# Performance work log

Measured on AMD Instinct MI355X. Metric: run time of the kernel, lower is better.

Reference implementation:

```python
import jax, jax.numpy as jnp
import numpy as np
import math

B, L, H, E, D = 4, 1024, 8, 64, 64


def setup_inputs() -> dict:
    key = jax.random.key(0)
    kq, kk, kv, ks = jax.random.split(key, 4)
    return {
        "queries": jax.random.normal(kq, (B, L, H, E), dtype=jnp.float32),
        "keys": jax.random.normal(kk, (B, L, H, E), dtype=jnp.float32),
        "values": jax.random.normal(kv, (B, L, H, D), dtype=jnp.float32),
        "sigma": jax.random.normal(ks, (B, L, H), dtype=jnp.float32),
    }


def reference(queries, keys, values, sigma):
    b, l, h, e = queries.shape
    scale = 1.0 / math.sqrt(e)

    # scores: [B, H, L, S]
    scores = jnp.einsum("blhe,bshe->bhls", queries, keys)

    # triangular causal mask (strict upper triangle -> -inf), applied BEFORE scaling
    causal = jnp.triu(jnp.ones((l, l), dtype=bool), k=1)  # [L, L]
    scores = jnp.where(causal[None, None], -jnp.inf, scores)
    attn = scale * scores

    # sigma branch: [B, L, H] -> [B, H, L], sigmoid/pow transform, broadcast over S
    sg = jax.nn.sigmoid(jnp.transpose(sigma, (0, 2, 1)) * 5.0) + 1e-5
    sg = jnp.power(3.0, sg) - 1.0          # [B, H, L]
    sg = sg[..., None]                      # [B, H, L, 1] (broadcast instead of tile)

    # Gaussian prior from |i - j| distances
    idx = jnp.arange(l, dtype=jnp.float32)
    dist = jnp.abs(idx[:, None] - idx[None, :])  # [L, L]
    prior = (1.0 / (math.sqrt(2.0 * math.pi) * sg)) * jnp.exp(-(dist ** 2) / (2.0 * sg ** 2))  # [B,H,L,L]

    series = jax.nn.softmax(attn, axis=-1)  # dropout rate 0.0 -> identity
    V = jnp.einsum("bhls,bshd->blhd", series, values)

    sigma_out = jnp.broadcast_to(sg, prior.shape)  # matches tf.tile semantics
    return (V, series, prior, sigma_out)
```

## Files before the change

kernel.cpp:

```cpp
#include <hip/hip_runtime.h>
#include <hip/hip_bf16.h>

#define NB 4
#define NL 1024
#define NH 8
#define NE 64
#define NPRIOR (NB * NH * NL)

typedef __bf16 bf16x8_t __attribute__((ext_vector_type(8)));
typedef __bf16 bf16x4_t __attribute__((ext_vector_type(4)));
typedef float f32x4_t __attribute__((ext_vector_type(4)));

__device__ __forceinline__ int kidx(int row, int col) {
    return (row << 6) + (col ^ ((row & 7) << 3));
}
__device__ __forceinline__ int pidx(int row, int col) {
    return (row << 10) + (col ^ ((row & 7) << 3));
}

#define BAR() do { asm volatile("s_waitcnt lgkmcnt(0)" ::: "memory"); \
                   __builtin_amdgcn_s_barrier();                      \
                   asm volatile("" ::: "memory"); } while (0)

__global__ __launch_bounds__(256) void fused_kernel(
    const float* __restrict__ Qg, const float* __restrict__ Kg,
    const float* __restrict__ Vg, const float* __restrict__ Sgm,
    float* __restrict__ outV, float* __restrict__ outSer,
    float* __restrict__ outP, float* __restrict__ outSig)
{
    __shared__ __bf16 Pl[32 * 1024];
    __shared__ __bf16 KV[64 * 64];
    __shared__ float rsum[4][16];
    __shared__ float rinvs[32];
    __shared__ float sgl[72], cstl[72], nil[72];

    const int bid = blockIdx.x;
    const int p  = bid & 31;
    const int jp = bid >> 5;
    const int h = p & 7, b = p >> 3;
    const int tid = threadIdx.x;
    const int lane = tid & 63, wave = tid >> 6;
    const int l16 = lane & 15, lq = lane >> 4;
    const int rg  = wave >> 1;
    const int nsb = (wave & 1) << 1;
    const int rowstride = NH * NE;

    const float* Qb = Qg + ((size_t)b * NL) * rowstride + h * NE;
    const float* Kb = Kg + ((size_t)b * NL) * rowstride + h * NE;
    const float* Vb = Vg + ((size_t)b * NL) * rowstride + h * NE;
    float* ser = outSer + ((size_t)p << 20);
    const float scale = 0.125f;

    if (tid < 72) {
        const int g = (bid << 6) + tid;
        if (g < NPRIOR) {
            const int i  = g & (NL - 1);
            const int ph = g >> 10;
            const float s   = Sgm[((size_t)(ph >> 3) * NL + i) * NH + (ph & 7)];
            const float sig = 1.f / (1.f + __expf(-5.f * s)) + 1e-5f;
            const float sg  = expm1f(sig * 1.0986122886681098f);
            sgl[tid]  = sg;
            cstl[tid] = 0.3989422804014327f / sg;
            nil[tid]  = -0.5f / (sg * sg);
        }
    }

    int prow = 0;
    auto emit4 = [&]() {
        #pragma unroll
        for (int c = 0; c < 4; ++c) {
            const int lr = prow + c;
            const int g  = (bid << 6) + lr;
            if (g < NPRIOR) {
                const int i  = g & (NL - 1);
                const int ph = g >> 10;
                const float sg  = sgl[lr];
                const float cst = cstl[lr];
                const float ni  = nil[lr];
                const size_t ob = ((size_t)ph << 20) + ((size_t)i << 10);
                const int j0 = tid << 2;
                const float fd = (float)(i - j0);
                f32x4_t pr;
                pr.x = cst * __expf(fd * fd * ni);
                const float f1 = fd - 1.f; pr.y = cst * __expf(f1 * f1 * ni);
                const float f2 = fd - 2.f; pr.z = cst * __expf(f2 * f2 * ni);
                const float f3 = fd - 3.f; pr.w = cst * __expf(f3 * f3 * ni);
                __builtin_nontemporal_store(pr, (f32x4_t*)(outP + ob + j0));
                f32x4_t sv = {sg, sg, sg, sg};
                __builtin_nontemporal_store(sv, (f32x4_t*)(outSig + ob + j0));
            }
        }
        prow += 4;
    };

    float4 kr[8];
    auto loadK = [&](int ct) {
        #pragma unroll
        for (int nn = 0; nn < 2; ++nn) {
            const float* row = Kb +
                (size_t)((ct << 6) + ((nsb + nn) << 4) + l16) * rowstride;
            kr[nn * 4 + 0] = *(const float4*)(row + (lq << 3));
            kr[nn * 4 + 1] = *(const float4*)(row + (lq << 3) + 4);
            kr[nn * 4 + 2] = *(const float4*)(row + 32 + (lq << 3));
            kr[nn * 4 + 3] = *(const float4*)(row + 32 + (lq << 3) + 4);
        }
    };

    float4 preV[4];
    auto loadV = [&](int ct) {
        const float* src = Vb + ((size_t)(ct << 6)) * rowstride;
        #pragma unroll
        for (int it = 0; it < 4; ++it) {
            int g = tid + (it << 8);
            int row = g >> 4, c4 = (g & 15) << 2;
            preV[it] = *(const float4*)(src + (size_t)row * rowstride + c4);
        }
    };
    auto writeVt = [&]() {
        #pragma unroll
        for (int it = 0; it < 4; ++it) {
            int g = tid + (it << 8);
            int row = g >> 4, c4 = (g & 15) << 2;
            KV[kidx(c4 + 0, row)] = (__bf16)preV[it].x;
            KV[kidx(c4 + 1, row)] = (__bf16)preV[it].y;
            KV[kidx(c4 + 2, row)] = (__bf16)preV[it].z;
            KV[kidx(c4 + 3, row)] = (__bf16)preV[it].w;
        }
    };

    auto do_tile = [&](int t) {
        const int r0  = t << 5;
        const int nct = (t + 2) >> 1;

        loadK(0);
        loadV(0);

        BAR();
        #pragma unroll
        for (int it = 0; it < 2; ++it) {
            int g = tid + (it << 8);
            int row = g >> 4, c4 = (g & 15) << 2;
            float4 v = *(const float4*)(Qb + (size_t)(r0 + row) * rowstride + c4);
            bf16x4_t w;
            w[0] = (__bf16)v.x; w[1] = (__bf16)v.y;
            w[2] = (__bf16)v.z; w[3] = (__bf16)v.w;
            *(bf16x4_t*)(KV + kidx(row, c4)) = w;
        }
        BAR();
        bf16x8_t qf0, qf1;
        {
            int row = (rg << 4) + l16;
            qf0 = *(bf16x8_t*)(KV + kidx(row, lq << 3));
            qf1 = *(bf16x8_t*)(KV + kidx(row, 32 + (lq << 3)));
        }

        const int qloc = (rg << 4) + l16;
        const int qg   = r0 + qloc;
        const int rloc0 = (rg << 4) + (lq << 2);

        float psum = 0.f;
        f32x4_t accO0 = {0.f, 0.f, 0.f, 0.f};
        f32x4_t accO1 = {0.f, 0.f, 0.f, 0.f};

        for (int ct = 0; ct < nct; ++ct) {
            BAR();
            writeVt();
            if (ct + 1 < nct) loadV(ct + 1);
            #pragma unroll
            for (int nn = 0; nn < 2; ++nn) {
                bf16x8_t a0, a1;
                {
                    float4 p0 = kr[nn * 4 + 0], p1 = kr[nn * 4 + 1];
                    float4 p2 = kr[nn * 4 + 2], p3 = kr[nn * 4 + 3];
                    a0[0] = (__bf16)p0.x; a0[1] = (__bf16)p0.y;
                    a0[2] = (__bf16)p0.z; a0[3] = (__bf16)p0.w;
                    a0[4] = (__bf16)p1.x; a0[5] = (__bf16)p1.y;
                    a0[6] = (__bf16)p1.z; a0[7] = (__bf16)p1.w;
                    a1[0] = (__bf16)p2.x; a1[1] = (__bf16)p2.y;
                    a1[2] = (__bf16)p2.z; a1[3] = (__bf16)p2.w;
                    a1[4] = (__bf16)p3.x; a1[5] = (__bf16)p3.y;
                    a1[6] = (__bf16)p3.z; a1[7] = (__bf16)p3.w;
                }
                f32x4_t acc = {0.f, 0.f, 0.f, 0.f};
                acc = __builtin_amdgcn_mfma_f32_16x16x32_bf16(a0, qf0, acc, 0, 0, 0);
                acc = __builtin_amdgcn_mfma_f32_16x16x32_bf16(a1, qf1, acc, 0, 0, 0);
                const int jbase = (ct << 6) + ((nsb + nn) << 4) + (lq << 2);
                bf16x4_t pw;
                #pragma unroll
                for (int r = 0; r < 4; ++r) {
                    float e = (jbase + r <= qg) ? __expf(acc[r] * scale) : 0.f;
                    psum += e;
                    pw[r] = (__bf16)e;
                }
                *(bf16x4_t*)(Pl + pidx(qloc, jbase)) = pw;
            }
            if (ct + 1 < nct) loadK(ct + 1);
            BAR();
            #pragma unroll
            for (int ks = 0; ks < 2; ++ks) {
                bf16x8_t pa = *(bf16x8_t*)(Pl + pidx((rg << 4) + l16,
                                             (ct << 6) + (ks << 5) + (lq << 3)));
                bf16x8_t vb0 = *(bf16x8_t*)(KV + kidx((nsb << 4) + l16,
                                             (ks << 5) + (lq << 3)));
                accO0 = __builtin_amdgcn_mfma_f32_16x16x32_bf16(pa, vb0, accO0, 0, 0, 0);
                bf16x8_t vb1 = *(bf16x8_t*)(KV + kidx(((nsb + 1) << 4) + l16,
                                             (ks << 5) + (lq << 3)));
                accO1 = __builtin_amdgcn_mfma_f32_16x16x32_bf16(pa, vb1, accO1, 0, 0, 0);
            }
            emit4();
        }

        {
            float s = psum;
            s += __shfl_xor(s, 16);
            s += __shfl_xor(s, 32);
            if (lane < 16) rsum[wave][l16] = s;
        }
        BAR();
        if (tid < 32) {
            int rgx = tid >> 4;
            float tot = rsum[rgx << 1][tid & 15] + rsum[(rgx << 1) | 1][tid & 15];
            rinvs[tid] = 1.f / tot;
        }
        BAR();

        #pragma unroll
        for (int r = 0; r < 4; ++r) {
            int rloc = rloc0 + r;
            float rv = rinvs[rloc];
            float* dst = outV + ((size_t)b * NL + r0 + rloc) * rowstride + h * NE;
            dst[(nsb << 4) + l16]       = accO0[r] * rv;
            dst[((nsb + 1) << 4) + l16] = accO1[r] * rv;
        }

        const int lim = nct << 6;
        #pragma unroll 2
        for (int rr = wave; rr < 32; rr += 4) {
            float rv = rinvs[rr];
            float* dst = ser + ((size_t)(r0 + rr) << 10);
            #pragma unroll
            for (int k = 0; k < 4; ++k) {
                int col = (lane << 2) + (k << 8);
                f32x4_t o;
                if (col < lim) {
                    bf16x4_t p4 = *(bf16x4_t*)(Pl + pidx(rr, col));
                    o.x = (float)p4[0] * rv;
                    o.y = (float)p4[1] * rv;
                    o.z = (float)p4[2] * rv;
                    o.w = (float)p4[3] * rv;
                } else {
                    o.x = 0.f; o.y = 0.f; o.z = 0.f; o.w = 0.f;
                }
                __builtin_nontemporal_store(o, (f32x4_t*)(dst + col));
            }
        }
    };

    do_tile(31 - jp);
    do_tile(jp);

    while (prow < 64) emit4();
}

extern "C" void kernel_launch(void* const* d_in, const int* in_sizes, int n_in,
                              void* d_out, int out_size, void* d_ws, size_t ws_size,
                              hipStream_t stream) {
    const float* Q  = (const float*)d_in[0];
    const float* K  = (const float*)d_in[1];
    const float* V  = (const float*)d_in[2];
    const float* Sg = (const float*)d_in[3];

    float* out      = (float*)d_out;
    float* outV     = out;
    float* outSer   = out + 2097152;
    float* outPrior = out + 35651584;
    float* outSig   = out + 69206016;

    hipLaunchKernelGGL(fused_kernel, dim3(512), dim3(256), 0, stream,
                       Q, K, V, Sg, outV, outSer, outPrior, outSig);
}
```

Measured before the change: 87.26 us.

## Split softmax into a row-sum pass and a streaming normalize pass to shrink LDS

A first pass computes only the softmax denominators with QK MFMAs. A second pass recomputes the scores and streams the normalized probabilities per 64-column tile straight to global memory. This removes the 64KB full-row P buffer in shared memory, which should allow more blocks per CU. The grid doubles to 1024 blocks with one 32-row tile each instead of paired tiles, and the prior/sigma rows are spread evenly across blocks. The cost is computing QK twice, and the per-block work is no longer balanced by the causal-pair trick.

```diff
diff --git a/kernel.cpp b/kernel.cpp
--- a/kernel.cpp
+++ b/kernel.cpp
@@ -14,8 +14,12 @@
 __device__ __forceinline__ int kidx(int row, int col) {
     return (row << 6) + (col ^ ((row & 7) << 3));
 }
-__device__ __forceinline__ int pidx(int row, int col) {
-    return (row << 10) + (col ^ ((row & 7) << 3));
+
+__device__ __forceinline__ bf16x8_t cvt8(const float4& a, const float4& b) {
+    bf16x8_t r;
+    r[0] = (__bf16)a.x; r[1] = (__bf16)a.y; r[2] = (__bf16)a.z; r[3] = (__bf16)a.w;
+    r[4] = (__bf16)b.x; r[5] = (__bf16)b.y; r[6] = (__bf16)b.z; r[7] = (__bf16)b.w;
+    return r;
 }
 
 #define BAR() do { asm volatile("s_waitcnt lgkmcnt(0)" ::: "memory"); \
@@ -28,15 +32,15 @@
     float* __restrict__ outV, float* __restrict__ outSer,
     float* __restrict__ outP, float* __restrict__ outSig)
 {
-    __shared__ __bf16 Pl[32 * 1024];
-    __shared__ __bf16 KV[64 * 64];
+    __shared__ __bf16 Vt[64 * 64];
+    __shared__ __bf16 Ps[32 * 64];
     __shared__ float rsum[4][16];
     __shared__ float rinvs[32];
-    __shared__ float sgl[72], cstl[72], nil[72];
+    __shared__ float sgl[32], cstl[32], nil[32];
 
     const int bid = blockIdx.x;
-    const int p  = bid & 31;
-    const int jp = bid >> 5;
+    const int p = bid & 31;
+    const int t = bid >> 5;
     const int h = p & 7, b = p >> 3;
     const int tid = threadIdx.x;
     const int lane = tid & 63, wave = tid >> 6;
@@ -50,61 +54,114 @@
     const float* Vb = Vg + ((size_t)b * NL) * rowstride + h * NE;
     float* ser = outSer + ((size_t)p << 20);
     const float scale = 0.125f;
-
-    if (tid < 72) {
-        const int g = (bid << 6) + tid;
-        if (g < NPRIOR) {
+    const int r0  = t << 5;
+    const int nct = (t + 2) >> 1;
+
+    if (tid < 32) {
+        const int g  = (bid << 5) + tid;
+        const int i  = g & (NL - 1);
+        const int ph = g >> 10;
+        const float s   = Sgm[((size_t)(ph >> 3) * NL + i) * NH + (ph & 7)];
+        const float sig = 1.f / (1.f + __expf(-5.f * s)) + 1e-5f;
+        const float sg  = expm1f(sig * 1.0986122886681098f);
+        sgl[tid]  = sg;
+        cstl[tid] = 0.3989422804014327f / sg;
+        nil[tid]  = -0.5f / (sg * sg);
+    }
+
+    int prow = 0;
+    auto emit2 = [&]() {
+        #pragma unroll
+        for (int c = 0; c < 2; ++c) {
+            const int lr = prow + c;
+            const int g  = (bid << 5) + lr;
             const int i  = g & (NL - 1);
             const int ph = g >> 10;
-            const float s   = Sgm[((size_t)(ph >> 3) * NL + i) * NH + (ph & 7)];
-            const float sig = 1.f / (1.f + __expf(-5.f * s)) + 1e-5f;
-            const float sg  = expm1f(sig * 1.0986122886681098f);
-            sgl[tid]  = sg;
-            cstl[tid] = 0.3989422804014327f / sg;
-            nil[tid]  = -0.5f / (sg * sg);
-        }
-    }
-
-    int prow = 0;
-    auto emit4 = [&]() {
-        #pragma unroll
-        for (int c = 0; c < 4; ++c) {
-            const int lr = prow + c;
-            const int g  = (bid << 6) + lr;
-            if (g < NPRIOR) {
-                const int i  = g & (NL - 1);
-                const int ph = g >> 10;
-                const float sg  = sgl[lr];
-                const float cst = cstl[lr];
-                const float ni  = nil[lr];
-                const size_t ob = ((size_t)ph << 20) + ((size_t)i << 10);
-                const int j0 = tid << 2;
-                const float fd = (float)(i - j0);
-                f32x4_t pr;
-                pr.x = cst * __expf(fd * fd * ni);
-                const float f1 = fd - 1.f; pr.y = cst * __expf(f1 * f1 * ni);
-                const float f2 = fd - 2.f; pr.z = cst * __expf(f2 * f2 * ni);
-                const float f3 = fd - 3.f; pr.w = cst * __expf(f3 * f3 * ni);
-                __builtin_nontemporal_store(pr, (f32x4_t*)(outP + ob + j0));
-                f32x4_t sv = {sg, sg, sg, sg};
-                __builtin_nontemporal_store(sv, (f32x4_t*)(outSig + ob + j0));
-            }
-        }
-        prow += 4;
-    };
-
-    float4 kr[8];
-    auto loadK = [&](int ct) {
+            const float sg  = sgl[lr];
+            const float cst = cstl[lr];
+            const float ni  = nil[lr];
+            const size_t ob = ((size_t)ph << 20) + ((size_t)i << 10);
+            const int j0 = tid << 2;
+            const float fd = (float)(i - j0);
+            f32x4_t pr;
+            pr.x = cst * __expf(fd * fd * ni);
+            const float f1 = fd - 1.f; pr.y = cst * __expf(f1 * f1 * ni);
+            const float f2 = fd - 2.f; pr.z = cst * __expf(f2 * f2 * ni);
+            const float f3 = fd - 3.f; pr.w = cst * __expf(f3 * f3 * ni);
+            __builtin_nontemporal_store(pr, (f32x4_t*)(outP + ob + j0));
+            f32x4_t sv = {sg, sg, sg, sg};
+            __builtin_nontemporal_store(sv, (f32x4_t*)(outSig + ob + j0));
+        }
+        prow += 2;
+    };
+
+    const int qloc = (rg << 4) + l16;
+    const int qg   = r0 + qloc;
+    bf16x8_t qf0, qf1;
+    {
+        const float* qr = Qb + (size_t)(r0 + qloc) * rowstride;
+        float4 a = *(const float4*)(qr + (lq << 3));
+        float4 c = *(const float4*)(qr + (lq << 3) + 4);
+        qf0 = cvt8(a, c);
+        float4 d = *(const float4*)(qr + 32 + (lq << 3));
+        float4 e = *(const float4*)(qr + 32 + (lq << 3) + 4);
+        qf1 = cvt8(d, e);
+    }
+
+    auto loadK = [&](int ct, bf16x8_t (&ka)[4]) {
         #pragma unroll
         for (int nn = 0; nn < 2; ++nn) {
-            const float* row = Kb +
+            const float* krow = Kb +
                 (size_t)((ct << 6) + ((nsb + nn) << 4) + l16) * rowstride;
-            kr[nn * 4 + 0] = *(const float4*)(row + (lq << 3));
-            kr[nn * 4 + 1] = *(const float4*)(row + (lq << 3) + 4);
-            kr[nn * 4 + 2] = *(const float4*)(row + 32 + (lq << 3));
-            kr[nn * 4 + 3] = *(const float4*)(row + 32 + (lq << 3) + 4);
-        }
-    };
+            float4 p0 = *(const float4*)(krow + (lq << 3));
+            float4 p1 = *(const float4*)(krow + (lq << 3) + 4);
+            float4 p2 = *(const float4*)(krow + 32 + (lq << 3));
+            float4 p3 = *(const float4*)(krow + 32 + (lq << 3) + 4);
+            ka[nn * 2 + 0] = cvt8(p0, p1);
+            ka[nn * 2 + 1] = cvt8(p2, p3);
+        }
+    };
+
+    auto qk_psum = [&](int ct, bf16x8_t (&ka)[4], float& ps) {
+        #pragma unroll
+        for (int nn = 0; nn < 2; ++nn) {
+            f32x4_t acc = {0.f, 0.f, 0.f, 0.f};
+            acc = __builtin_amdgcn_mfma_f32_16x16x32_bf16(ka[nn * 2 + 0], qf0, acc, 0, 0, 0);
+            acc = __builtin_amdgcn_mfma_f32_16x16x32_bf16(ka[nn * 2 + 1], qf1, acc, 0, 0, 0);
+            const int jb = (ct << 6) + ((nsb + nn) << 4) + (lq << 2);
+            #pragma unroll
+            for (int r = 0; r < 4; ++r)
+                if (jb + r <= qg) ps += __expf(acc[r] * scale);
+        }
+    };
+
+    float psum = 0.f;
+    {
+        bf16x8_t kA[4], kB[4];
+        loadK(0, kA);
+        #pragma unroll 1
+        for (int ct = 0; ct < nct; ct += 2) {
+            if (ct + 1 < nct) loadK(ct + 1, kB);
+            qk_psum(ct, kA, psum);
+            if (ct + 1 < nct) {
+                if (ct + 2 < nct) loadK(ct + 2, kA);
+                qk_psum(ct + 1, kB, psum);
+            }
+        }
+    }
+    psum += __shfl_xor(psum, 16);
+    psum += __shfl_xor(psum, 32);
+    if (lane < 16) rsum[wave][l16] = psum;
+    BAR();
+    if (tid < 32) {
+        const int rgx = tid >> 4;
+        float tot = rsum[rgx << 1][tid & 15] + rsum[(rgx << 1) | 1][tid & 15];
+        rinvs[tid] = 1.f / tot;
+    }
+    BAR();
+
+    f32x4_t accO0 = {0.f, 0.f, 0.f, 0.f};
+    f32x4_t accO1 = {0.f, 0.f, 0.f, 0.f};
 
     float4 preV[4];
     auto loadV = [&](int ct) {
@@ -121,145 +178,84 @@
         for (int it = 0; it < 4; ++it) {
             int g = tid + (it << 8);
             int row = g >> 4, c4 = (g & 15) << 2;
-            KV[kidx(c4 + 0, row)] = (__bf16)preV[it].x;
-            KV[kidx(c4 + 1, row)] = (__bf16)preV[it].y;
-            KV[kidx(c4 + 2, row)] = (__bf16)preV[it].z;
-            KV[kidx(c4 + 3, row)] = (__bf16)preV[it].w;
-        }
-    };
-
-    auto do_tile = [&](int t) {
-        const int r0  = t << 5;
-        const int nct = (t + 2) >> 1;
-
-        loadK(0);
-        loadV(0);
-
-        BAR();
-        #pragma unroll
-        for (int it = 0; it < 2; ++it) {
-            int g = tid + (it << 8);
-            int row = g >> 4, c4 = (g & 15) << 2;
-            float4 v = *(const float4*)(Qb + (size_t)(r0 + row) * rowstride + c4);
-            bf16x4_t w;
-            w[0] = (__bf16)v.x; w[1] = (__bf16)v.y;
-            w[2] = (__bf16)v.z; w[3] = (__bf16)v.w;
-            *(bf16x4_t*)(KV + kidx(row, c4)) = w;
-        }
-        BAR();
-        bf16x8_t qf0, qf1;
-        {
-            int row = (rg << 4) + l16;
-            qf0 = *(bf16x8_t*)(KV + kidx(row, lq << 3));
-            qf1 = *(bf16x8_t*)(KV + kidx(row, 32 + (lq << 3)));
-        }
-
-        const int qloc = (rg << 4) + l16;
-        const int qg   = r0 + qloc;
-        const int rloc0 = (rg << 4) + (lq << 2);
-
-        float psum = 0.f;
-        f32x4_t accO0 = {0.f, 0.f, 0.f, 0.f};
-        f32x4_t accO1 = {0.f, 0.f, 0.f, 0.f};
-
-        for (int ct = 0; ct < nct; ++ct) {
+            Vt[kidx(c4 + 0, row)] = (__bf16)preV[it].x;
+            Vt[kidx(c4 + 1, row)] = (__bf16)preV[it].y;
+            Vt[kidx(c4 + 2, row)] = (__bf16)preV[it].z;
+            Vt[kidx(c4 + 3, row)] = (__bf16)preV[it].w;
+        }
+    };
+
+    bf16x8_t kc[4];
+    loadK(0, kc);
+    loadV(0);
+
+    const int srow = tid >> 3;
+    const int scol = (tid & 7) << 3;
+
+    #pragma unroll 1
+    for (int ct = 0; ct < 16; ++ct) {
+        if (ct < nct) {
             BAR();
             writeVt();
             if (ct + 1 < nct) loadV(ct + 1);
             #pragma unroll
             for (int nn = 0; nn < 2; ++nn) {
-                bf16x8_t a0, a1;
-                {
-                    float4 p0 = kr[nn * 4 + 0], p1 = kr[nn * 4 + 1];
-                    float4 p2 = kr[nn * 4 + 2], p3 = kr[nn * 4 + 3];
-                    a0[0] = (__bf16)p0.x; a0[1] = (__bf16)p0.y;
-                    a0[2] = (__bf16)p0.z; a0[3] = (__bf16)p0.w;
-                    a0[4] = (__bf16)p1.x; a0[5] = (__bf16)p1.y;
-                    a0[6] = (__bf16)p1.z; a0[7] = (__bf16)p1.w;
-                    a1[0] = (__bf16)p2.x; a1[1] = (__bf16)p2.y;
-                    a1[2] = (__bf16)p2.z; a1[3] = (__bf16)p2.w;
-                    a1[4] = (__bf16)p3.x; a1[5] = (__bf16)p3.y;
-                    a1[6] = (__bf16)p3.z; a1[7] = (__bf16)p3.w;
-                }
                 f32x4_t acc = {0.f, 0.f, 0.f, 0.f};
-                acc = __builtin_amdgcn_mfma_f32_16x16x32_bf16(a0, qf0, acc, 0, 0, 0);
-                acc = __builtin_amdgcn_mfma_f32_16x16x32_bf16(a1, qf1, acc, 0, 0, 0);
-                const int jbase = (ct << 6) + ((nsb + nn) << 4) + (lq << 2);
+                acc = __builtin_amdgcn_mfma_f32_16x16x32_bf16(kc[nn * 2 + 0], qf0, acc, 0, 0, 0);
+                acc = __builtin_amdgcn_mfma_f32_16x16x32_bf16(kc[nn * 2 + 1], qf1, acc, 0, 0, 0);
+                const int jb  = (ct << 6) + ((nsb + nn) << 4) + (lq << 2);
+                const int jbl = ((nsb + nn) << 4) + (lq << 2);
                 bf16x4_t pw;
                 #pragma unroll
                 for (int r = 0; r < 4; ++r) {
-                    float e = (jbase + r <= qg) ? __expf(acc[r] * scale) : 0.f;
-                    psum += e;
+                    float e = (jb + r <= qg) ? __expf(acc[r] * scale) : 0.f;
                     pw[r] = (__bf16)e;
                 }
-                *(bf16x4_t*)(Pl + pidx(qloc, jbase)) = pw;
-            }
-            if (ct + 1 < nct) loadK(ct + 1);
+                *(bf16x4_t*)(Ps + kidx(qloc, jbl)) = pw;
+            }
+            if (ct + 1 < nct) loadK(ct + 1, kc);
             BAR();
             #pragma unroll
             for (int ks = 0; ks < 2; ++ks) {
-                bf16x8_t pa = *(bf16x8_t*)(Pl + pidx((rg << 4) + l16,
-                                             (ct << 6) + (ks << 5) + (lq << 3)));
-                bf16x8_t vb0 = *(bf16x8_t*)(KV + kidx((nsb << 4) + l16,
-                                             (ks << 5) + (lq << 3)));
+                bf16x8_t pa = *(bf16x8_t*)(Ps + kidx((rg << 4) + l16,
+                                                     (ks << 5) + (lq << 3)));
+                bf16x8_t vb0 = *(bf16x8_t*)(Vt + kidx((nsb << 4) + l16,
+                                                      (ks << 5) + (lq << 3)));
                 accO0 = __builtin_amdgcn_mfma_f32_16x16x32_bf16(pa, vb0, accO0, 0, 0, 0);
-                bf16x8_t vb1 = *(bf16x8_t*)(KV + kidx(((nsb + 1) << 4) + l16,
-                                             (ks << 5) + (lq << 3)));
+                bf16x8_t vb1 = *(bf16x8_t*)(Vt + kidx(((nsb + 1) << 4) + l16,
+                                                      (ks << 5) + (lq << 3)));
                 accO1 = __builtin_amdgcn_mfma_f32_16x16x32_bf16(pa, vb1, accO1, 0, 0, 0);
             }
-            emit4();
-        }
-
-        {
-            float s = psum;
-            s += __shfl_xor(s, 16);
-            s += __shfl_xor(s, 32);
-            if (lane < 16) rsum[wave][l16] = s;
-        }
-        BAR();
-        if (tid < 32) {
-            int rgx = tid >> 4;
-            float tot = rsum[rgx << 1][tid & 15] + rsum[(rgx << 1) | 1][tid & 15];
-            rinvs[tid] = 1.f / tot;
-        }
-        BAR();
-
-        #pragma unroll
-        for (int r = 0; r < 4; ++r) {
-            int rloc = rloc0 + r;
-            float rv = rinvs[rloc];
-            float* dst = outV + ((size_t)b * NL + r0 + rloc) * rowstride + h * NE;
-            dst[(nsb << 4) + l16]       = accO0[r] * rv;
-            dst[((nsb + 1) << 4) + l16] = accO1[r] * rv;
-        }
-
-        const int lim = nct << 6;
-        #pragma unroll 2
-        for (int rr = wave; rr < 32; rr += 4) {
-            float rv = rinvs[rr];
-            float* dst = ser + ((size_t)(r0 + rr) << 10);
-            #pragma unroll
-            for (int k = 0; k < 4; ++k) {
-                int col = (lane << 2) + (k << 8);
-                f32x4_t o;
-                if (col < lim) {
-                    bf16x4_t p4 = *(bf16x4_t*)(Pl + pidx(rr, col));
-                    o.x = (float)p4[0] * rv;
-                    o.y = (float)p4[1] * rv;
-                    o.z = (float)p4[2] * rv;
-                    o.w = (float)p4[3] * rv;
-                } else {
-                    o.x = 0.f; o.y = 0.f; o.z = 0.f; o.w = 0.f;
-                }
-                __builtin_nontemporal_store(o, (f32x4_t*)(dst + col));
-            }
-        }
-    };
-
-    do_tile(31 - jp);
-    do_tile(jp);
-
-    while (prow < 64) emit4();
+            {
+                bf16x8_t p8 = *(bf16x8_t*)(Ps + kidx(srow, scol));
+                const float rv = rinvs[srow];
+                float* dst = ser + ((size_t)(r0 + srow) << 10) + (ct << 6) + scol;
+                f32x4_t o0, o1;
+                o0.x = (float)p8[0] * rv; o0.y = (float)p8[1] * rv;
+                o0.z = (float)p8[2] * rv; o0.w = (float)p8[3] * rv;
+                o1.x = (float)p8[4] * rv; o1.y = (float)p8[5] * rv;
+                o1.z = (float)p8[6] * rv; o1.w = (float)p8[7] * rv;
+                __builtin_nontemporal_store(o0, (f32x4_t*)dst);
+                __builtin_nontemporal_store(o1, (f32x4_t*)(dst + 4));
+            }
+        } else {
+            float* dst = ser + ((size_t)(r0 + srow) << 10) + (ct << 6) + scol;
+            f32x4_t z = {0.f, 0.f, 0.f, 0.f};
+            __builtin_nontemporal_store(z, (f32x4_t*)dst);
+            __builtin_nontemporal_store(z, (f32x4_t*)(dst + 4));
+        }
+        emit2();
+    }
+
+    const int rloc0 = (rg << 4) + (lq << 2);
+    #pragma unroll
+    for (int r = 0; r < 4; ++r) {
+        const int rloc = rloc0 + r;
+        const float rv = rinvs[rloc];
+        float* dst = outV + ((size_t)b * NL + r0 + rloc) * rowstride + h * NE;
+        dst[(nsb << 4) + l16]       = accO0[r] * rv;
+        dst[((nsb + 1) << 4) + l16] = accO1[r] * rv;
+    }
 }
 
 extern "C" void kernel_launch(void* const* d_in, const int* in_sizes, int n_in,
@@ -276,6 +272,6 @@
     float* outPrior = out + 35651584;
     float* outSig   = out + 69206016;
 
-    hipLaunchKernelGGL(fused_kernel, dim3(512), dim3(256), 0, stream,
+    hipLaunchKernelGGL(fused_kernel, dim3(1024), dim3(256), 0, stream,
                        Q, K, V, Sg, outV, outSer, outPrior, outSig);
 }
```

Result: slower. 136.5 us (+56.4%).
